# Kernel tuning notes

Measured on AMD Instinct MI355X. Metric: run time of the kernel, lower is better.

Reference implementation:

```python
import jax, jax.numpy as jnp
import numpy as np

N_NODES = 100000
N_EDGES = 800000
N_GRAPHS = 128
BN_EPS = 1e-5


def _bn(h, g, b, m, v):
    # BatchNorm1d in eval mode: uses running stats
    return (h - m) * jax.lax.rsqrt(v + BN_EPS) * g + b


def _gin_layer(x, edge_index, eps, wa, ba, g, be, m, v, wb, bb):
    src, dst = edge_index[0], edge_index[1]
    # sparse neighbor sum: scatter-add messages x[src] into dst
    agg = jax.ops.segment_sum(x[src], dst, num_segments=N_NODES)
    h = (1.0 + eps) * x + agg  # eps shape [1] broadcasts
    h = jax.nn.relu(_bn(h @ wa + ba, g, be, m, v))
    return jax.nn.relu(h @ wb + bb)


def setup_inputs() -> dict:
    key = jax.random.key(0)
    ks = jax.random.split(key, 12)
    inp = {
        'x': jax.random.normal(ks[0], (N_NODES, 384), dtype=jnp.float32),
        'edge_index': jax.random.randint(ks[1], (2, N_EDGES), 0, N_NODES, dtype=jnp.int64),
        'batch': jnp.sort(jax.random.randint(ks[2], (N_NODES,), 0, N_GRAPHS, dtype=jnp.int64)),
        'eps1': jnp.zeros((1,), jnp.float32),
        'w1a': jax.random.normal(ks[3], (384, 128), jnp.float32) * 0.05,
        'b1a': jnp.zeros((128,), jnp.float32),
        'g1': jnp.ones((128,), jnp.float32), 'be1': jnp.zeros((128,), jnp.float32),
        'm1': jnp.zeros((128,), jnp.float32), 'v1': jnp.ones((128,), jnp.float32),
        'w1b': jax.random.normal(ks[4], (128, 128), jnp.float32) * 0.05,
        'b1b': jnp.zeros((128,), jnp.float32),
        'eps2': jnp.zeros((1,), jnp.float32),
        'w2a': jax.random.normal(ks[5], (128, 128), jnp.float32) * 0.05,
        'b2a': jnp.zeros((128,), jnp.float32),
        'g2': jnp.ones((128,), jnp.float32), 'be2': jnp.zeros((128,), jnp.float32),
        'm2': jnp.zeros((128,), jnp.float32), 'v2': jnp.ones((128,), jnp.float32),
        'w2b': jax.random.normal(ks[6], (128, 128), jnp.float32) * 0.05,
        'b2b': jnp.zeros((128,), jnp.float32),
        'eps3': jnp.zeros((1,), jnp.float32),
        'w3a': jax.random.normal(ks[7], (128, 128), jnp.float32) * 0.05,
        'b3a': jnp.zeros((128,), jnp.float32),
        'g3': jnp.ones((128,), jnp.float32), 'be3': jnp.zeros((128,), jnp.float32),
        'm3': jnp.zeros((128,), jnp.float32), 'v3': jnp.ones((128,), jnp.float32),
        'w3b': jax.random.normal(ks[8], (128, 64), jnp.float32) * 0.05,
        'b3b': jnp.zeros((64,), jnp.float32),
        'wc': jax.random.normal(ks[9], (64, 2), jnp.float32) * 0.05,
        'bc': jnp.zeros((2,), jnp.float32),
    }
    return inp


def reference(x, edge_index, batch,
              eps1, w1a, b1a, g1, be1, m1, v1, w1b, b1b,
              eps2, w2a, b2a, g2, be2, m2, v2, w2b, b2b,
              eps3, w3a, b3a, g3, be3, m3, v3, w3b, b3b,
              wc, bc):
    h = _gin_layer(x, edge_index, eps1, w1a, b1a, g1, be1, m1, v1, w1b, b1b)
    # dropout is identity in eval mode
    h = _gin_layer(h, edge_index, eps2, w2a, b2a, g2, be2, m2, v2, w2b, b2b)
    h = _gin_layer(h, edge_index, eps3, w3a, b3a, g3, be3, m3, v3, w3b, b3b)
    # global add pool over graphs
    pooled = jax.ops.segment_sum(h, batch, num_segments=N_GRAPHS)  # [G, 64]
    return pooled @ wc + bc  # [G, num_classes]
```

## Files before the change

### kernel.cpp

```cpp
#include <hip/hip_runtime.h>
#include <hip/hip_bf16.h>


#define N_NODES 100000
#define N_EDGES 800000
#define N_GRAPHS 128
#define NB_SCAN 391
#define LDP 136
#define FLDP 68
#define G1_BLOCKS 1563
#define HIST_BLOCKS 782

typedef __bf16 bf16x8 __attribute__((ext_vector_type(8)));
typedef float f32x4 __attribute__((ext_vector_type(4)));
typedef unsigned short ushort_t;
typedef unsigned int uint_t;

static __device__ __forceinline__ ushort_t f2b(float f) {
    uint_t u = __builtin_bit_cast(uint_t, f);
    uint_t r = (u + 0x7fffu + ((u >> 16) & 1u)) >> 16;
    return (ushort_t)r;
}
static __device__ __forceinline__ float b2f(ushort_t u) {
    return __builtin_bit_cast(float, (uint_t)u << 16);
}

__global__ __launch_bounds__(256) void wt_all_k(
        const float* __restrict__ w1a, const float* __restrict__ w1b,
        const float* __restrict__ w2a, const float* __restrict__ w2b,
        const float* __restrict__ w3a, const float* __restrict__ w3b,
        ushort_t* __restrict__ o1a, ushort_t* __restrict__ o1b,
        ushort_t* __restrict__ o2a, ushort_t* __restrict__ o2b,
        ushort_t* __restrict__ o3a, ushort_t* __restrict__ o3b,
        int* __restrict__ ideg, float* __restrict__ pooled) {
    int t = blockIdx.x * 256 + threadIdx.x;
    if (t < 122880) {
        const float* W; ushort_t* O; int K, N, i;
        if      (t <  49152) { W = w1a; O = o1a; K = 384; N = 128; i = t; }
        else if (t <  65536) { W = w1b; O = o1b; K = 128; N = 128; i = t - 49152; }
        else if (t <  81920) { W = w2a; O = o2a; K = 128; N = 128; i = t - 65536; }
        else if (t <  98304) { W = w2b; O = o2b; K = 128; N = 128; i = t - 81920; }
        else if (t < 114688) { W = w3a; O = o3a; K = 128; N = 128; i = t - 98304; }
        else                 { W = w3b; O = o3b; K = 128; N = 64;  i = t - 114688; }
        int k = i / N, c = i % N;
        O[c * K + k] = f2b(W[i]);
    } else if (t < 222880) {
        ideg[t - 122880] = 0;
    } else if (t < 231072) {
        pooled[t - 222880] = 0.f;
    }
}

__global__ __launch_bounds__(256) void gemm1_hist_k(const float* __restrict__ A,
                                                    const ushort_t* __restrict__ Wt,
                                                    ushort_t* __restrict__ C, int M,
                                                    const int* __restrict__ dst,
                                                    int* __restrict__ deg) {
    __shared__ ushort_t Al[64 * LDP];

    if (blockIdx.x >= G1_BLOCKS) {
        int b = blockIdx.x - G1_BLOCKS;
        int e0 = b * 1024 + threadIdx.x;
        #pragma unroll
        for (int p = 0; p < 4; ++p) {
            int e = e0 + p * 256;
            if (e < N_EDGES) atomicAdd(&deg[dst[e]], 1);
        }
        return;
    }

    constexpr int K = 384;
    const int tid  = threadIdx.x;
    const int lane = tid & 63;
    const int wid  = tid >> 6;
    const int wrow = wid >> 1;
    const int wcol = wid & 1;
    const int l15  = lane & 15;
    const int kg   = lane >> 4;
    const int row0 = blockIdx.x * 64;

    f32x4 acc[2][4];
    #pragma unroll
    for (int i = 0; i < 2; ++i)
        #pragma unroll
        for (int j = 0; j < 4; ++j)
            acc[i][j] = f32x4{0.f, 0.f, 0.f, 0.f};

    const int r  = tid >> 2;
    const int cc = (tid & 3) * 32;

    for (int k0 = 0; k0 < K; k0 += 128) {
        __syncthreads();
        {
            int gr = row0 + r;
            if (gr > M - 1) gr = M - 1;
            const float* pA = A + (size_t)gr * K + k0 + cc;
            float4 v[8];
            #pragma unroll
            for (int p = 0; p < 8; ++p)
                v[p] = *reinterpret_cast<const float4*>(pA + p * 4);
            uint_t u[16];
            #pragma unroll
            for (int p = 0; p < 8; ++p) {
                u[2 * p]     = (uint_t)f2b(v[p].x) | ((uint_t)f2b(v[p].y) << 16);
                u[2 * p + 1] = (uint_t)f2b(v[p].z) | ((uint_t)f2b(v[p].w) << 16);
            }
            uint4* dstp = reinterpret_cast<uint4*>(&Al[r * LDP + cc]);
            dstp[0] = make_uint4(u[0], u[1], u[2], u[3]);
            dstp[1] = make_uint4(u[4], u[5], u[6], u[7]);
            dstp[2] = make_uint4(u[8], u[9], u[10], u[11]);
            dstp[3] = make_uint4(u[12], u[13], u[14], u[15]);
        }
        __syncthreads();

        #pragma unroll
        for (int kk = 0; kk < 4; ++kk) {
            bf16x8 a0 = *reinterpret_cast<const bf16x8*>(&Al[(wrow * 32 + l15) * LDP + kk * 32 + kg * 8]);
            bf16x8 a1 = *reinterpret_cast<const bf16x8*>(&Al[(wrow * 32 + 16 + l15) * LDP + kk * 32 + kg * 8]);
            #pragma unroll
            for (int j = 0; j < 4; ++j) {
                int col = wcol * 64 + j * 16 + l15;
                bf16x8 b = *reinterpret_cast<const bf16x8*>(Wt + (size_t)col * K + k0 + kk * 32 + kg * 8);
                acc[0][j] = __builtin_amdgcn_mfma_f32_16x16x32_bf16(a0, b, acc[0][j], 0, 0, 0);
                acc[1][j] = __builtin_amdgcn_mfma_f32_16x16x32_bf16(a1, b, acc[1][j], 0, 0, 0);
            }
        }
    }

    __syncthreads();
    #pragma unroll
    for (int i = 0; i < 2; ++i)
        #pragma unroll
        for (int j = 0; j < 4; ++j) {
            int col = wcol * 64 + j * 16 + l15;
            #pragma unroll
            for (int q = 0; q < 4; ++q) {
                int row = wrow * 32 + i * 16 + kg * 4 + q;
                Al[row * LDP + col] = f2b(acc[i][j][q]);
            }
        }
    __syncthreads();
    #pragma unroll
    for (int p = 0; p < 4; ++p) {
        int idx = tid + p * 256;
        int rr = idx >> 4, c16 = idx & 15;
        int gr = row0 + rr;
        if (gr < M)
            *reinterpret_cast<uint4*>(C + (size_t)gr * 128 + c16 * 8) =
                *reinterpret_cast<const uint4*>(&Al[rr * LDP + c16 * 8]);
    }
}

__global__ __launch_bounds__(256) void scan1_k(const int* __restrict__ deg,
                                               int* __restrict__ tmp,
                                               int* __restrict__ bsum) {
    __shared__ int s[256];
    int i = blockIdx.x * 256 + threadIdx.x;
    int t = threadIdx.x;
    s[t] = (i < N_NODES) ? deg[i] : 0;
    __syncthreads();
    for (int off = 1; off < 256; off <<= 1) {
        int v = (t >= off) ? s[t - off] : 0;
        __syncthreads();
        s[t] += v;
        __syncthreads();
    }
    if (i < N_NODES) tmp[i] = s[t];
    if (t == 255) bsum[blockIdx.x] = s[255];
}

__global__ __launch_bounds__(256) void scan23_k(const int* __restrict__ tmp,
                                                const int* __restrict__ deg,
                                                const int* __restrict__ bsum,
                                                int* __restrict__ row_start) {
    __shared__ int sb[256];
    int t = threadIdx.x;
    int partial = 0;
    for (int i = t; i < (int)blockIdx.x; i += 256) partial += bsum[i];
    sb[t] = partial;
    __syncthreads();
    for (int off = 128; off > 0; off >>= 1) {
        if (t < off) sb[t] += sb[t + off];
        __syncthreads();
    }
    int boff = sb[0];
    int i = blockIdx.x * 256 + t;
    if (i < N_NODES) row_start[i] = tmp[i] - deg[i] + boff;
}

__global__ __launch_bounds__(256) void fill_k(const int* __restrict__ src,
                                              const int* __restrict__ dst,
                                              int* __restrict__ row_start,
                                              int* __restrict__ csr_src) {
    int e = blockIdx.x * 256 + threadIdx.x;
    if (e >= N_EDGES) return;
    int idx = atomicAdd(&row_start[dst[e]], 1);
    csr_src[idx] = src[e];
}

template<bool TAIL>
__global__ __launch_bounds__(256) void gather_mlp_k(
        const ushort_t* __restrict__ Yin,
        const int* __restrict__ csr, const int* __restrict__ rend,
        const int* __restrict__ deg,
        const float* __restrict__ epsp, const float* __restrict__ ba,
        const float* __restrict__ g, const float* __restrict__ be,
        const float* __restrict__ mm, const float* __restrict__ vv,
        const ushort_t* __restrict__ Wb, const float* __restrict__ bias1,
        const ushort_t* __restrict__ Wa2,
        ushort_t* __restrict__ Yout,
        const int* __restrict__ batch, float* __restrict__ pooled, int M) {
    constexpr int NJ1 = TAIL ? 2 : 4;
    __shared__ ushort_t Hl[64 * LDP];
    __shared__ ushort_t Xl[64 * LDP];
    float* Fl = (float*)Xl;

    const int tid  = threadIdx.x;
    const int lane = tid & 63;
    const int wid  = tid >> 6;
    const int l15  = lane & 15;
    const int slot = lane >> 4;
    const int c0   = l15 * 8;
    const int row0 = blockIdx.x * 64;

    {
        float ep = 1.0f + epsp[0];
        float sc[8], sh[8];
        #pragma unroll
        for (int jj = 0; jj < 8; ++jj) {
            int c = c0 + jj;
            float s = g[c] * rsqrtf(vv[c] + 1e-5f);
            sc[jj] = s;
            sh[jj] = (ba[c] - mm[c]) * s + be[c];
        }

        const int base = row0 + wid * 16;
        int cn = base; if (cn > M - 1) cn = M - 1;
        int end = rend[cn], d = deg[cn];
        int st = end - d;
        int nlim = (d > 64) ? 64 : d;
        int nb = (lane < nlim) ? csr[st + lane] : 0;

        for (int nl = 0; nl < 16; ++nl) {
            int node = base + nl; if (node > M - 1) node = M - 1;
            int nxt = base + nl + 1; if (nxt > M - 1) nxt = M - 1;
            int nend = 0, nd = 0;
            if (nl < 15) { nend = rend[nxt]; nd = deg[nxt]; }

            uint4 ow = *reinterpret_cast<const uint4*>(Yin + (size_t)node * 128 + c0);

            float acc[8] = {0.f, 0.f, 0.f, 0.f, 0.f, 0.f, 0.f, 0.f};
            for (int j0 = 0; j0 < nlim; j0 += 8) {
                int jA = j0 + slot;
                int jB = j0 + 4 + slot;
                int ia = __shfl(nb, jA & 63);
                int ib = __shfl(nb, jB & 63);
                uint4 wa = *reinterpret_cast<const uint4*>(Yin + (size_t)ia * 128 + c0);
                uint4 wb = *reinterpret_cast<const uint4*>(Yin + (size_t)ib * 128 + c0);
                float fa = (jA < nlim) ? 1.f : 0.f;
                float fb = (jB < nlim) ? 1.f : 0.f;
                uint_t ua[4] = {wa.x, wa.y, wa.z, wa.w};
                uint_t ub[4] = {wb.x, wb.y, wb.z, wb.w};
                #pragma unroll
                for (int p = 0; p < 4; ++p) {
                    acc[2 * p]     += fa * b2f((ushort_t)(ua[p] & 0xffff));
                    acc[2 * p + 1] += fa * b2f((ushort_t)(ua[p] >> 16));
                    acc[2 * p]     += fb * b2f((ushort_t)(ub[p] & 0xffff));
                    acc[2 * p + 1] += fb * b2f((ushort_t)(ub[p] >> 16));
                }
            }
            for (int j = st + 64; j < end; ++j) {
                if (slot == 0) {
                    int idx = csr[j];
                    uint4 w = *reinterpret_cast<const uint4*>(Yin + (size_t)idx * 128 + c0);
                    uint_t uw[4] = {w.x, w.y, w.z, w.w};
                    #pragma unroll
                    for (int p = 0; p < 4; ++p) {
                        acc[2 * p]     += b2f((ushort_t)(uw[p] & 0xffff));
                        acc[2 * p + 1] += b2f((ushort_t)(uw[p] >> 16));
                    }
                }
            }

            int nst = nend - nd;
            int nnlim = (nd > 64) ? 64 : nd;
            int nb2 = 0;
            if (nl < 15 && lane < nnlim) nb2 = csr[nst + lane];

            #pragma unroll
            for (int jj = 0; jj < 8; ++jj) {
                acc[jj] += __shfl_xor(acc[jj], 16);
                acc[jj] += __shfl_xor(acc[jj], 32);
            }
            uint_t uo[4] = {ow.x, ow.y, ow.z, ow.w};
            ushort_t rr[8];
            #pragma unroll
            for (int p = 0; p < 4; ++p) {
                float o0 = b2f((ushort_t)(uo[p] & 0xffff));
                float o1 = b2f((ushort_t)(uo[p] >> 16));
                float t0 = sc[2 * p] * (ep * o0 + acc[2 * p]) + sh[2 * p];
                float t1 = sc[2 * p + 1] * (ep * o1 + acc[2 * p + 1]) + sh[2 * p + 1];
                rr[2 * p]     = f2b(fmaxf(t0, 0.f));
                rr[2 * p + 1] = f2b(fmaxf(t1, 0.f));
            }
            if (slot == 0) {
                uint4 packed;
                packed.x = (uint_t)rr[0] | ((uint_t)rr[1] << 16);
                packed.y = (uint_t)rr[2] | ((uint_t)rr[3] << 16);
                packed.z = (uint_t)rr[4] | ((uint_t)rr[5] << 16);
                packed.w = (uint_t)rr[6] | ((uint_t)rr[7] << 16);
                *reinterpret_cast<uint4*>(&Hl[(wid * 16 + nl) * LDP + c0]) = packed;
            }

            end = nend; d = nd; st = nst; nlim = nnlim; nb = nb2;
        }
    }
    __syncthreads();

    const int wrow = wid >> 1;
    const int wcol = wid & 1;
    const int kg   = lane >> 4;

    f32x4 acc1[2][NJ1];
    #pragma unroll
    for (int i = 0; i < 2; ++i)
        #pragma unroll
        for (int j = 0; j < NJ1; ++j)
            acc1[i][j] = f32x4{0.f, 0.f, 0.f, 0.f};
    #pragma unroll
    for (int kk = 0; kk < 4; ++kk) {
        bf16x8 a0 = *reinterpret_cast<const bf16x8*>(&Hl[(wrow * 32 + l15) * LDP + kk * 32 + kg * 8]);
        bf16x8 a1 = *reinterpret_cast<const bf16x8*>(&Hl[(wrow * 32 + 16 + l15) * LDP + kk * 32 + kg * 8]);
        #pragma unroll
        for (int j = 0; j < NJ1; ++j) {
            int col = wcol * (16 * NJ1) + j * 16 + l15;
            bf16x8 b = *reinterpret_cast<const bf16x8*>(Wb + (size_t)col * 128 + kk * 32 + kg * 8);
            acc1[0][j] = __builtin_amdgcn_mfma_f32_16x16x32_bf16(a0, b, acc1[0][j], 0, 0, 0);
            acc1[1][j] = __builtin_amdgcn_mfma_f32_16x16x32_bf16(a1, b, acc1[1][j], 0, 0, 0);
        }
    }

    if constexpr (TAIL) {
        #pragma unroll
        for (int i = 0; i < 2; ++i)
            #pragma unroll
            for (int j = 0; j < NJ1; ++j) {
                int col = wcol * 32 + j * 16 + l15;
                float bi = bias1[col];
                #pragma unroll
                for (int q = 0; q < 4; ++q) {
                    int row = wrow * 32 + i * 16 + kg * 4 + q;
                    Fl[row * FLDP + col] = fmaxf(acc1[i][j][q] + bi, 0.f);
                }
            }
        __syncthreads();
        int col = tid & 63;
        int qq  = tid >> 6;
        float a = 0.f;
        int cur = -1;
        for (int rr2 = 0; rr2 < 16; ++rr2) {
            int r = qq * 16 + rr2;
            int gr = row0 + r;
            if (gr >= M) break;
            int b = batch[gr];
            if (b != cur) {
                if (cur >= 0) atomicAdd(&pooled[cur * 64 + col], a);
                a = 0.f;
                cur = b;
            }
            a += Fl[r * FLDP + col];
        }
        if (cur >= 0) atomicAdd(&pooled[cur * 64 + col], a);
    } else {
        #pragma unroll
        for (int i = 0; i < 2; ++i)
            #pragma unroll
            for (int j = 0; j < NJ1; ++j) {
                int col = wcol * 64 + j * 16 + l15;
                float bi = bias1[col];
                #pragma unroll
                for (int q = 0; q < 4; ++q) {
                    int row = wrow * 32 + i * 16 + kg * 4 + q;
                    Xl[row * LDP + col] = f2b(fmaxf(acc1[i][j][q] + bi, 0.f));
                }
            }
        __syncthreads();

        f32x4 acc2[2][4];
        #pragma unroll
        for (int i = 0; i < 2; ++i)
            #pragma unroll
            for (int j = 0; j < 4; ++j)
                acc2[i][j] = f32x4{0.f, 0.f, 0.f, 0.f};
        #pragma unroll
        for (int kk = 0; kk < 4; ++kk) {
            bf16x8 a0 = *reinterpret_cast<const bf16x8*>(&Xl[(wrow * 32 + l15) * LDP + kk * 32 + kg * 8]);
            bf16x8 a1 = *reinterpret_cast<const bf16x8*>(&Xl[(wrow * 32 + 16 + l15) * LDP + kk * 32 + kg * 8]);
            #pragma unroll
            for (int j = 0; j < 4; ++j) {
                int col = wcol * 64 + j * 16 + l15;
                bf16x8 b = *reinterpret_cast<const bf16x8*>(Wa2 + (size_t)col * 128 + kk * 32 + kg * 8);
                acc2[0][j] = __builtin_amdgcn_mfma_f32_16x16x32_bf16(a0, b, acc2[0][j], 0, 0, 0);
                acc2[1][j] = __builtin_amdgcn_mfma_f32_16x16x32_bf16(a1, b, acc2[1][j], 0, 0, 0);
            }
        }
        __syncthreads();
        #pragma unroll
        for (int i = 0; i < 2; ++i)
            #pragma unroll
            for (int j = 0; j < 4; ++j) {
                int col = wcol * 64 + j * 16 + l15;
                #pragma unroll
                for (int q = 0; q < 4; ++q) {
                    int row = wrow * 32 + i * 16 + kg * 4 + q;
                    Hl[row * LDP + col] = f2b(acc2[i][j][q]);
                }
            }
        __syncthreads();
        #pragma unroll
        for (int p = 0; p < 4; ++p) {
            int idx = tid + p * 256;
            int r = idx >> 4, c16 = idx & 15;
            int gr = row0 + r;
            if (gr < M)
                *reinterpret_cast<uint4*>(Yout + (size_t)gr * 128 + c16 * 8) =
                    *reinterpret_cast<const uint4*>(&Hl[r * LDP + c16 * 8]);
        }
    }
}

__global__ __launch_bounds__(256) void classifier_k(const float* __restrict__ pooled,
                                                    const float* __restrict__ wc,
                                                    const float* __restrict__ bc,
                                                    float* __restrict__ out) {
    int t = threadIdx.x;
    int gidx = t >> 1, c = t & 1;
    float s = bc[c];
    #pragma unroll
    for (int k = 0; k < 64; ++k)
        s += pooled[gidx * 64 + k] * wc[k * 2 + c];
    out[gidx * 2 + c] = s;
}

extern "C" void kernel_launch(void* const* d_in, const int* in_sizes, int n_in,
                              void* d_out, int out_size, void* d_ws, size_t ws_size,
                              hipStream_t stream) {
    const float* x     = (const float*)d_in[0];
    const int*   ei    = (const int*)d_in[1];
    const int*   src   = ei;
    const int*   dst   = ei + N_EDGES;
    const int*   batch = (const int*)d_in[2];
    const float* eps1 = (const float*)d_in[3];
    const float* w1a  = (const float*)d_in[4];
    const float* b1a  = (const float*)d_in[5];
    const float* g1   = (const float*)d_in[6];
    const float* be1  = (const float*)d_in[7];
    const float* m1   = (const float*)d_in[8];
    const float* v1   = (const float*)d_in[9];
    const float* w1b  = (const float*)d_in[10];
    const float* b1b  = (const float*)d_in[11];
    const float* eps2 = (const float*)d_in[12];
    const float* w2a  = (const float*)d_in[13];
    const float* b2a  = (const float*)d_in[14];
    const float* g2   = (const float*)d_in[15];
    const float* be2  = (const float*)d_in[16];
    const float* m2   = (const float*)d_in[17];
    const float* v2   = (const float*)d_in[18];
    const float* w2b  = (const float*)d_in[19];
    const float* b2b  = (const float*)d_in[20];
    const float* eps3 = (const float*)d_in[21];
    const float* w3a  = (const float*)d_in[22];
    const float* b3a  = (const float*)d_in[23];
    const float* g3   = (const float*)d_in[24];
    const float* be3  = (const float*)d_in[25];
    const float* m3   = (const float*)d_in[26];
    const float* v3   = (const float*)d_in[27];
    const float* w3b  = (const float*)d_in[28];
    const float* b3b  = (const float*)d_in[29];
    const float* wc   = (const float*)d_in[30];
    const float* bc   = (const float*)d_in[31];
    float* out = (float*)d_out;

    ushort_t* Y = (ushort_t*)d_ws;
    ushort_t* H = Y + 12800000;
    ushort_t* wt1a = H + 12800000;
    ushort_t* wt1b = wt1a + 49152;
    ushort_t* wt2a = wt1b + 16384;
    ushort_t* wt2b = wt2a + 16384;
    ushort_t* wt3a = wt2b + 16384;
    ushort_t* wt3b = wt3a + 16384;
    float* pooled = (float*)(wt3b + 8192);
    int* ideg = (int*)(pooled + 8192);
    int* irow = ideg + N_NODES;
    int* itmp = irow + N_NODES;
    int* icsr = itmp + N_NODES;
    int* ibsum = icsr + N_EDGES;

    const int M = N_NODES;
    const int gGemm = (M + 63) / 64;
    const int gEdge = (N_EDGES + 255) / 256;
    const int gNode = NB_SCAN;

    wt_all_k<<<903, 256, 0, stream>>>(w1a, w1b, w2a, w2b, w3a, w3b,
                                      wt1a, wt1b, wt2a, wt2b, wt3a, wt3b,
                                      ideg, pooled);

    gemm1_hist_k<<<G1_BLOCKS + HIST_BLOCKS, 256, 0, stream>>>(x, wt1a, Y, M, dst, ideg);

    scan1_k<<<gNode, 256, 0, stream>>>(ideg, itmp, ibsum);
    scan23_k<<<gNode, 256, 0, stream>>>(itmp, ideg, ibsum, irow);
    fill_k<<<gEdge, 256, 0, stream>>>(src, dst, irow, icsr);

    gather_mlp_k<false><<<gGemm, 256, 0, stream>>>(
        Y, icsr, irow, ideg, eps1, b1a, g1, be1, m1, v1,
        wt1b, b1b, wt2a, H, nullptr, nullptr, M);
    gather_mlp_k<false><<<gGemm, 256, 0, stream>>>(
        H, icsr, irow, ideg, eps2, b2a, g2, be2, m2, v2,
        wt2b, b2b, wt3a, Y, nullptr, nullptr, M);
    gather_mlp_k<true><<<gGemm, 256, 0, stream>>>(
        Y, icsr, irow, ideg, eps3, b3a, g3, be3, m3, v3,
        wt3b, b3b, nullptr, nullptr, batch, pooled, M);

    classifier_k<<<1, 256, 0, stream>>>(pooled, wc, bc, out);
}
```

Measured before the change: 359.1 us.

## Double-buffer gemm1 A tiles with async global-to-LDS loads and swizzle

The first-layer GEMM now streams fp32 A tiles straight into LDS with global_load_lds, double-buffered over six 64-wide K steps, so the next tile's load overlaps the current MFMA work. Conversion to bf16 moves to the LDS read side, and an XOR swizzle on 16-byte chunks is meant to avoid bank conflicts. The goal is to hide global load latency and drop the register round trip and one barrier per step. In exchange LDS use doubles (fp32, two buffers), which may lower occupancy, and each wave repeats the fp32-to-bf16 conversions on every LDS read.

```diff
diff --git a/kernel.cpp b/kernel.cpp
--- a/kernel.cpp
+++ b/kernel.cpp
@@ -23,6 +23,12 @@
 }
 static __device__ __forceinline__ float b2f(ushort_t u) {
     return __builtin_bit_cast(float, (uint_t)u << 16);
+}
+
+static __device__ __forceinline__ void gload_lds16(const float* gp, float* lp) {
+    __builtin_amdgcn_global_load_lds(
+        (const __attribute__((address_space(1))) void*)gp,
+        (__attribute__((address_space(3))) void*)lp, 16, 0, 0);
 }
 
 __global__ __launch_bounds__(256) void wt_all_k(
@@ -56,7 +62,7 @@
                                                     ushort_t* __restrict__ C, int M,
                                                     const int* __restrict__ dst,
                                                     int* __restrict__ deg) {
-    __shared__ ushort_t Al[64 * LDP];
+    __shared__ float Af[2][64 * 64];
 
     if (blockIdx.x >= G1_BLOCKS) {
         int b = blockIdx.x - G1_BLOCKS;
@@ -79,6 +85,16 @@
     const int kg   = lane >> 4;
     const int row0 = blockIdx.x * 64;
 
+    const int Rb = wid * 4 + (lane >> 4);
+    int grs[4]; int css[4];
+    #pragma unroll
+    for (int p = 0; p < 4; ++p) {
+        int R = p * 16 + Rb;
+        int gr = row0 + R; if (gr > M - 1) gr = M - 1;
+        grs[p] = gr;
+        css[p] = (lane & 15) ^ (R & 7);
+    }
+
     f32x4 acc[2][4];
     #pragma unroll
     for (int i = 0; i < 2; ++i)
@@ -86,48 +102,53 @@
         for (int j = 0; j < 4; ++j)
             acc[i][j] = f32x4{0.f, 0.f, 0.f, 0.f};
 
-    const int r  = tid >> 2;
-    const int cc = (tid & 3) * 32;
-
-    for (int k0 = 0; k0 < K; k0 += 128) {
-        __syncthreads();
-        {
-            int gr = row0 + r;
-            if (gr > M - 1) gr = M - 1;
-            const float* pA = A + (size_t)gr * K + k0 + cc;
-            float4 v[8];
-            #pragma unroll
-            for (int p = 0; p < 8; ++p)
-                v[p] = *reinterpret_cast<const float4*>(pA + p * 4);
-            uint_t u[16];
-            #pragma unroll
-            for (int p = 0; p < 8; ++p) {
-                u[2 * p]     = (uint_t)f2b(v[p].x) | ((uint_t)f2b(v[p].y) << 16);
-                u[2 * p + 1] = (uint_t)f2b(v[p].z) | ((uint_t)f2b(v[p].w) << 16);
-            }
-            uint4* dstp = reinterpret_cast<uint4*>(&Al[r * LDP + cc]);
-            dstp[0] = make_uint4(u[0], u[1], u[2], u[3]);
-            dstp[1] = make_uint4(u[4], u[5], u[6], u[7]);
-            dstp[2] = make_uint4(u[8], u[9], u[10], u[11]);
-            dstp[3] = make_uint4(u[12], u[13], u[14], u[15]);
-        }
-        __syncthreads();
-
-        #pragma unroll
-        for (int kk = 0; kk < 4; ++kk) {
-            bf16x8 a0 = *reinterpret_cast<const bf16x8*>(&Al[(wrow * 32 + l15) * LDP + kk * 32 + kg * 8]);
-            bf16x8 a1 = *reinterpret_cast<const bf16x8*>(&Al[(wrow * 32 + 16 + l15) * LDP + kk * 32 + kg * 8]);
+    #pragma unroll
+    for (int p = 0; p < 4; ++p)
+        gload_lds16(A + (size_t)grs[p] * K + 0 + css[p] * 4,
+                    &Af[0][p * 1024 + wid * 256]);
+    __syncthreads();
+
+    int cur = 0;
+    const int rA0 = wrow * 32 + l15;
+    const int rA1 = wrow * 32 + 16 + l15;
+    const int s0 = rA0 & 7, s1 = rA1 & 7;
+
+    #pragma unroll
+    for (int t = 0; t < 6; ++t) {
+        if (t < 5) {
+            int k0n = (t + 1) * 64;
+            #pragma unroll
+            for (int p = 0; p < 4; ++p)
+                gload_lds16(A + (size_t)grs[p] * K + k0n + css[p] * 4,
+                            &Af[cur ^ 1][p * 1024 + wid * 256]);
+        }
+        const float* B0 = &Af[cur][rA0 * 64];
+        const float* B1 = &Af[cur][rA1 * 64];
+        #pragma unroll
+        for (int kk = 0; kk < 2; ++kk) {
+            int u0 = kk * 8 + kg * 2;
+            float4 lo0 = *reinterpret_cast<const float4*>(B0 + ((u0) ^ s0) * 4);
+            float4 hi0 = *reinterpret_cast<const float4*>(B0 + ((u0 + 1) ^ s0) * 4);
+            float4 lo1 = *reinterpret_cast<const float4*>(B1 + ((u0) ^ s1) * 4);
+            float4 hi1 = *reinterpret_cast<const float4*>(B1 + ((u0 + 1) ^ s1) * 4);
+            bf16x8 a0, a1;
+            a0[0] = (__bf16)lo0.x; a0[1] = (__bf16)lo0.y; a0[2] = (__bf16)lo0.z; a0[3] = (__bf16)lo0.w;
+            a0[4] = (__bf16)hi0.x; a0[5] = (__bf16)hi0.y; a0[6] = (__bf16)hi0.z; a0[7] = (__bf16)hi0.w;
+            a1[0] = (__bf16)lo1.x; a1[1] = (__bf16)lo1.y; a1[2] = (__bf16)lo1.z; a1[3] = (__bf16)lo1.w;
+            a1[4] = (__bf16)hi1.x; a1[5] = (__bf16)hi1.y; a1[6] = (__bf16)hi1.z; a1[7] = (__bf16)hi1.w;
             #pragma unroll
             for (int j = 0; j < 4; ++j) {
                 int col = wcol * 64 + j * 16 + l15;
-                bf16x8 b = *reinterpret_cast<const bf16x8*>(Wt + (size_t)col * K + k0 + kk * 32 + kg * 8);
+                bf16x8 b = *reinterpret_cast<const bf16x8*>(Wt + (size_t)col * K + t * 64 + kk * 32 + kg * 8);
                 acc[0][j] = __builtin_amdgcn_mfma_f32_16x16x32_bf16(a0, b, acc[0][j], 0, 0, 0);
                 acc[1][j] = __builtin_amdgcn_mfma_f32_16x16x32_bf16(a1, b, acc[1][j], 0, 0, 0);
             }
         }
-    }
-
-    __syncthreads();
+        __syncthreads();
+        cur ^= 1;
+    }
+
+    ushort_t* Es = (ushort_t*)&Af[0][0];
     #pragma unroll
     for (int i = 0; i < 2; ++i)
         #pragma unroll
@@ -136,7 +157,7 @@
             #pragma unroll
             for (int q = 0; q < 4; ++q) {
                 int row = wrow * 32 + i * 16 + kg * 4 + q;
-                Al[row * LDP + col] = f2b(acc[i][j][q]);
+                Es[row * LDP + col] = f2b(acc[i][j][q]);
             }
         }
     __syncthreads();
@@ -147,7 +168,7 @@
         int gr = row0 + rr;
         if (gr < M)
             *reinterpret_cast<uint4*>(C + (size_t)gr * 128 + c16 * 8) =
-                *reinterpret_cast<const uint4*>(&Al[rr * LDP + c16 * 8]);
+                *reinterpret_cast<const uint4*>(&Es[rr * LDP + c16 * 8]);
     }
 }
 
```

Measured after the change: 353.7 us. No clear change (-1.5%).

## Stream fp32 GEMM1 input directly to LDS and use 512-thread gather blocks

Applied to the files above, without the earlier changes.

The first-layer GEMM now loads the fp32 input tile straight into LDS with global_load_lds. It uses 32-row tiles with an XOR swizzle and converts to bf16 when building MFMA operands, instead of converting in registers before the LDS store. This aims to cut register pressure and VGPR round-trips on the bandwidth-heavy 384-wide input read, at the cost of twice as many blocks, each doing half the MFMA work per B-fragment load. The gather/MLP kernels move to 512-thread blocks with 8 nodes per wave instead of 16, raising wave-level parallelism for the irregular neighbour gathers. Each wave now holds 16 rows instead of 32 in its MFMA tiles, which lowers reuse of the weight fragments it loads.

```diff
diff --git a/kernel.cpp b/kernel.cpp
--- a/kernel.cpp
+++ b/kernel.cpp
@@ -8,7 +8,7 @@
 #define NB_SCAN 391
 #define LDP 136
 #define FLDP 68
-#define G1_BLOCKS 1563
+#define G1_BLOCKS 3125
 #define HIST_BLOCKS 782
 
 typedef __bf16 bf16x8 __attribute__((ext_vector_type(8)));
@@ -23,6 +23,12 @@
 }
 static __device__ __forceinline__ float b2f(ushort_t u) {
     return __builtin_bit_cast(float, (uint_t)u << 16);
+}
+
+static __device__ __forceinline__ void gload16(const void* gp, void* lp) {
+    __builtin_amdgcn_global_load_lds(
+        (const __attribute__((address_space(1))) void*)gp,
+        (__attribute__((address_space(3))) void*)lp, 16, 0, 0);
 }
 
 __global__ __launch_bounds__(256) void wt_all_k(
@@ -56,7 +62,7 @@
                                                     ushort_t* __restrict__ C, int M,
                                                     const int* __restrict__ dst,
                                                     int* __restrict__ deg) {
-    __shared__ ushort_t Al[64 * LDP];
+    __shared__ __align__(16) float Al[32 * 384];
 
     if (blockIdx.x >= G1_BLOCKS) {
         int b = blockIdx.x - G1_BLOCKS;
@@ -77,77 +83,62 @@
     const int wcol = wid & 1;
     const int l15  = lane & 15;
     const int kg   = lane >> 4;
-    const int row0 = blockIdx.x * 64;
-
-    f32x4 acc[2][4];
-    #pragma unroll
-    for (int i = 0; i < 2; ++i)
-        #pragma unroll
-        for (int j = 0; j < 4; ++j)
-            acc[i][j] = f32x4{0.f, 0.f, 0.f, 0.f};
-
-    const int r  = tid >> 2;
-    const int cc = (tid & 3) * 32;
-
-    for (int k0 = 0; k0 < K; k0 += 128) {
-        __syncthreads();
-        {
-            int gr = row0 + r;
-            if (gr > M - 1) gr = M - 1;
-            const float* pA = A + (size_t)gr * K + k0 + cc;
-            float4 v[8];
-            #pragma unroll
-            for (int p = 0; p < 8; ++p)
-                v[p] = *reinterpret_cast<const float4*>(pA + p * 4);
-            uint_t u[16];
-            #pragma unroll
-            for (int p = 0; p < 8; ++p) {
-                u[2 * p]     = (uint_t)f2b(v[p].x) | ((uint_t)f2b(v[p].y) << 16);
-                u[2 * p + 1] = (uint_t)f2b(v[p].z) | ((uint_t)f2b(v[p].w) << 16);
-            }
-            uint4* dstp = reinterpret_cast<uint4*>(&Al[r * LDP + cc]);
-            dstp[0] = make_uint4(u[0], u[1], u[2], u[3]);
-            dstp[1] = make_uint4(u[4], u[5], u[6], u[7]);
-            dstp[2] = make_uint4(u[8], u[9], u[10], u[11]);
-            dstp[3] = make_uint4(u[12], u[13], u[14], u[15]);
-        }
-        __syncthreads();
-
-        #pragma unroll
-        for (int kk = 0; kk < 4; ++kk) {
-            bf16x8 a0 = *reinterpret_cast<const bf16x8*>(&Al[(wrow * 32 + l15) * LDP + kk * 32 + kg * 8]);
-            bf16x8 a1 = *reinterpret_cast<const bf16x8*>(&Al[(wrow * 32 + 16 + l15) * LDP + kk * 32 + kg * 8]);
-            #pragma unroll
-            for (int j = 0; j < 4; ++j) {
-                int col = wcol * 64 + j * 16 + l15;
-                bf16x8 b = *reinterpret_cast<const bf16x8*>(Wt + (size_t)col * K + k0 + kk * 32 + kg * 8);
-                acc[0][j] = __builtin_amdgcn_mfma_f32_16x16x32_bf16(a0, b, acc[0][j], 0, 0, 0);
-                acc[1][j] = __builtin_amdgcn_mfma_f32_16x16x32_bf16(a1, b, acc[1][j], 0, 0, 0);
-            }
-        }
-    }
-
+    const int row0 = blockIdx.x * 32;
+
+    #pragma unroll
+    for (int p = 0; p < 12; ++p) {
+        int unit = tid + p * 256;
+        int r  = unit / 96;
+        int cu = unit % 96;
+        int cs = cu ^ (r & 7);
+        gload16(A + (size_t)(row0 + r) * K + cs * 4, &Al[unit * 4]);
+    }
     __syncthreads();
-    #pragma unroll
-    for (int i = 0; i < 2; ++i)
+
+    f32x4 acc[4];
+    #pragma unroll
+    for (int j = 0; j < 4; ++j) acc[j] = f32x4{0.f, 0.f, 0.f, 0.f};
+
+    const int rA = wrow * 16 + l15;
+    const int sw = rA & 7;
+    const float* Arow = &Al[rA * 384];
+
+    #pragma unroll
+    for (int kk = 0; kk < 12; ++kk) {
+        int u = kk * 8 + kg * 2;
+        float4 lo = *reinterpret_cast<const float4*>(Arow + ((u)     ^ sw) * 4);
+        float4 hi = *reinterpret_cast<const float4*>(Arow + ((u + 1) ^ sw) * 4);
+        bf16x8 a;
+        a[0] = (__bf16)lo.x; a[1] = (__bf16)lo.y; a[2] = (__bf16)lo.z; a[3] = (__bf16)lo.w;
+        a[4] = (__bf16)hi.x; a[5] = (__bf16)hi.y; a[6] = (__bf16)hi.z; a[7] = (__bf16)hi.w;
         #pragma unroll
         for (int j = 0; j < 4; ++j) {
             int col = wcol * 64 + j * 16 + l15;
-            #pragma unroll
-            for (int q = 0; q < 4; ++q) {
-                int row = wrow * 32 + i * 16 + kg * 4 + q;
-                Al[row * LDP + col] = f2b(acc[i][j][q]);
-            }
-        }
+            bf16x8 b = *reinterpret_cast<const bf16x8*>(Wt + (size_t)col * K + kk * 32 + kg * 8);
+            acc[j] = __builtin_amdgcn_mfma_f32_16x16x32_bf16(a, b, acc[j], 0, 0, 0);
+        }
+    }
+
     __syncthreads();
-    #pragma unroll
-    for (int p = 0; p < 4; ++p) {
+    ushort_t* Es = (ushort_t*)Al;
+    #pragma unroll
+    for (int j = 0; j < 4; ++j) {
+        int col = wcol * 64 + j * 16 + l15;
+        #pragma unroll
+        for (int q = 0; q < 4; ++q) {
+            int row = wrow * 16 + kg * 4 + q;
+            Es[row * LDP + col] = f2b(acc[j][q]);
+        }
+    }
+    __syncthreads();
+    #pragma unroll
+    for (int p = 0; p < 2; ++p) {
         int idx = tid + p * 256;
         int rr = idx >> 4, c16 = idx & 15;
         int gr = row0 + rr;
         if (gr < M)
             *reinterpret_cast<uint4*>(C + (size_t)gr * 128 + c16 * 8) =
-                *reinterpret_cast<const uint4*>(&Al[rr * LDP + c16 * 8]);
+                *reinterpret_cast<const uint4*>(&Es[rr * LDP + c16 * 8]);
     }
 }
 
@@ -199,7 +190,7 @@
 }
 
 template<bool TAIL>
-__global__ __launch_bounds__(256) void gather_mlp_k(
+__global__ __launch_bounds__(512) void gather_mlp_k(
         const ushort_t* __restrict__ Yin,
         const int* __restrict__ csr, const int* __restrict__ rend,
         const int* __restrict__ deg,
@@ -234,18 +225,18 @@
             sh[jj] = (ba[c] - mm[c]) * s + be[c];
         }
 
-        const int base = row0 + wid * 16;
+        const int base = row0 + wid * 8;
         int cn = base; if (cn > M - 1) cn = M - 1;
         int end = rend[cn], d = deg[cn];
         int st = end - d;
         int nlim = (d > 64) ? 64 : d;
         int nb = (lane < nlim) ? csr[st + lane] : 0;
 
-        for (int nl = 0; nl < 16; ++nl) {
+        for (int nl = 0; nl < 8; ++nl) {
             int node = base + nl; if (node > M - 1) node = M - 1;
             int nxt = base + nl + 1; if (nxt > M - 1) nxt = M - 1;
             int nend = 0, nd = 0;
-            if (nl < 15) { nend = rend[nxt]; nd = deg[nxt]; }
+            if (nl < 7) { nend = rend[nxt]; nd = deg[nxt]; }
 
             uint4 ow = *reinterpret_cast<const uint4*>(Yin + (size_t)node * 128 + c0);
 
@@ -285,7 +276,7 @@
             int nst = nend - nd;
             int nnlim = (nd > 64) ? 64 : nd;
             int nb2 = 0;
-            if (nl < 15 && lane < nnlim) nb2 = csr[nst + lane];
+            if (nl < 7 && lane < nnlim) nb2 = csr[nst + lane];
 
             #pragma unroll
             for (int jj = 0; jj < 8; ++jj) {
@@ -309,7 +300,7 @@
                 packed.y = (uint_t)rr[2] | ((uint_t)rr[3] << 16);
                 packed.z = (uint_t)rr[4] | ((uint_t)rr[5] << 16);
                 packed.w = (uint_t)rr[6] | ((uint_t)rr[7] << 16);
-                *reinterpret_cast<uint4*>(&Hl[(wid * 16 + nl) * LDP + c0]) = packed;
+                *reinterpret_cast<uint4*>(&Hl[(wid * 8 + nl) * LDP + c0]) = packed;
             }
 
             end = nend; d = nd; st = nst; nlim = nnlim; nb = nb2;
@@ -321,45 +312,38 @@
     const int wcol = wid & 1;
     const int kg   = lane >> 4;
 
-    f32x4 acc1[2][NJ1];
-    #pragma unroll
-    for (int i = 0; i < 2; ++i)
-        #pragma unroll
-        for (int j = 0; j < NJ1; ++j)
-            acc1[i][j] = f32x4{0.f, 0.f, 0.f, 0.f};
+    f32x4 acc1[NJ1];
+    #pragma unroll
+    for (int j = 0; j < NJ1; ++j) acc1[j] = f32x4{0.f, 0.f, 0.f, 0.f};
     #pragma unroll
     for (int kk = 0; kk < 4; ++kk) {
-        bf16x8 a0 = *reinterpret_cast<const bf16x8*>(&Hl[(wrow * 32 + l15) * LDP + kk * 32 + kg * 8]);
-        bf16x8 a1 = *reinterpret_cast<const bf16x8*>(&Hl[(wrow * 32 + 16 + l15) * LDP + kk * 32 + kg * 8]);
+        bf16x8 a = *reinterpret_cast<const bf16x8*>(&Hl[(wrow * 16 + l15) * LDP + kk * 32 + kg * 8]);
         #pragma unroll
         for (int j = 0; j < NJ1; ++j) {
             int col = wcol * (16 * NJ1) + j * 16 + l15;
             bf16x8 b = *reinterpret_cast<const bf16x8*>(Wb + (size_t)col * 128 + kk * 32 + kg * 8);
-            acc1[0][j] = __builtin_amdgcn_mfma_f32_16x16x32_bf16(a0, b, acc1[0][j], 0, 0, 0);
-            acc1[1][j] = __builtin_amdgcn_mfma_f32_16x16x32_bf16(a1, b, acc1[1][j], 0, 0, 0);
+            acc1[j] = __builtin_amdgcn_mfma_f32_16x16x32_bf16(a, b, acc1[j], 0, 0, 0);
         }
     }
 
     if constexpr (TAIL) {
         #pragma unroll
-        for (int i = 0; i < 2; ++i)
+        for (int j = 0; j < NJ1; ++j) {
+            int col = wcol * 32 + j * 16 + l15;
+            float bi = bias1[col];
             #pragma unroll
-            for (int j = 0; j < NJ1; ++j) {
-                int col = wcol * 32 + j * 16 + l15;
-                float bi = bias1[col];
-                #pragma unroll
-                for (int q = 0; q < 4; ++q) {
-                    int row = wrow * 32 + i * 16 + kg * 4 + q;
-                    Fl[row * FLDP + col] = fmaxf(acc1[i][j][q] + bi, 0.f);
-                }
-            }
+            for (int q = 0; q < 4; ++q) {
+                int row = wrow * 16 + kg * 4 + q;
+                Fl[row * FLDP + col] = fmaxf(acc1[j][q] + bi, 0.f);
+            }
+        }
         __syncthreads();
         int col = tid & 63;
         int qq  = tid >> 6;
         float a = 0.f;
         int cur = -1;
-        for (int rr2 = 0; rr2 < 16; ++rr2) {
-            int r = qq * 16 + rr2;
+        for (int rr2 = 0; rr2 < 8; ++rr2) {
+            int r = qq * 8 + rr2;
             int gr = row0 + r;
             if (gr >= M) break;
             int b = batch[gr];
@@ -373,53 +357,44 @@
         if (cur >= 0) atomicAdd(&pooled[cur * 64 + col], a);
     } else {
         #pragma unroll
-        for (int i = 0; i < 2; ++i)
+        for (int j = 0; j < NJ1; ++j) {
+            int col = wcol * 64 + j * 16 + l15;
+            float bi = bias1[col];
             #pragma unroll
-            for (int j = 0; j < NJ1; ++j) {
-                int col = wcol * 64 + j * 16 + l15;
-                float bi = bias1[col];
-                #pragma unroll
-                for (int q = 0; q < 4; ++q) {
-                    int row = wrow * 32 + i * 16 + kg * 4 + q;
-                    Xl[row * LDP + col] = f2b(fmaxf(acc1[i][j][q] + bi, 0.f));
-                }
-            }
-        __syncthreads();
-
-        f32x4 acc2[2][4];
-        #pragma unroll
-        for (int i = 0; i < 2; ++i)
-            #pragma unroll
-            for (int j = 0; j < 4; ++j)
-                acc2[i][j] = f32x4{0.f, 0.f, 0.f, 0.f};
+            for (int q = 0; q < 4; ++q) {
+                int row = wrow * 16 + kg * 4 + q;
+                Xl[row * LDP + col] = f2b(fmaxf(acc1[j][q] + bi, 0.f));
+            }
+        }
+        __syncthreads();
+
+        f32x4 acc2[4];
+        #pragma unroll
+        for (int j = 0; j < 4; ++j) acc2[j] = f32x4{0.f, 0.f, 0.f, 0.f};
         #pragma unroll
         for (int kk = 0; kk < 4; ++kk) {
-            bf16x8 a0 = *reinterpret_cast<const bf16x8*>(&Xl[(wrow * 32 + l15) * LDP + kk * 32 + kg * 8]);
-            bf16x8 a1 = *reinterpret_cast<const bf16x8*>(&Xl[(wrow * 32 + 16 + l15) * LDP + kk * 32 + kg * 8]);
+            bf16x8 a = *reinterpret_cast<const bf16x8*>(&Xl[(wrow * 16 + l15) * LDP + kk * 32 + kg * 8]);
             #pragma unroll
             for (int j = 0; j < 4; ++j) {
                 int col = wcol * 64 + j * 16 + l15;
                 bf16x8 b = *reinterpret_cast<const bf16x8*>(Wa2 + (size_t)col * 128 + kk * 32 + kg * 8);
-                acc2[0][j] = __builtin_amdgcn_mfma_f32_16x16x32_bf16(a0, b, acc2[0][j], 0, 0, 0);
-                acc2[1][j] = __builtin_amdgcn_mfma_f32_16x16x32_bf16(a1, b, acc2[1][j], 0, 0, 0);
-            }
-        }
-        __syncthreads();
-        #pragma unroll
-        for (int i = 0; i < 2; ++i)
+                acc2[j] = __builtin_amdgcn_mfma_f32_16x16x32_bf16(a, b, acc2[j], 0, 0, 0);
+            }
+        }
+        __syncthreads();
+        #pragma unroll
+        for (int j = 0; j < 4; ++j) {
+            int col = wcol * 64 + j * 16 + l15;
             #pragma unroll
-            for (int j = 0; j < 4; ++j) {
-                int col = wcol * 64 + j * 16 + l15;
-                #pragma unroll
-                for (int q = 0; q < 4; ++q) {
-                    int row = wrow * 32 + i * 16 + kg * 4 + q;
-                    Hl[row * LDP + col] = f2b(acc2[i][j][q]);
-                }
-            }
-        __syncthreads();
-        #pragma unroll
-        for (int p = 0; p < 4; ++p) {
-            int idx = tid + p * 256;
+            for (int q = 0; q < 4; ++q) {
+                int row = wrow * 16 + kg * 4 + q;
+                Hl[row * LDP + col] = f2b(acc2[j][q]);
+            }
+        }
+        __syncthreads();
+        #pragma unroll
+        for (int p = 0; p < 2; ++p) {
+            int idx = tid + p * 512;
             int r = idx >> 4, c16 = idx & 15;
             int gr = row0 + r;
             if (gr < M)
@@ -497,7 +472,7 @@
     int* ibsum = icsr + N_EDGES;
 
     const int M = N_NODES;
-    const int gGemm = (M + 63) / 64;
+    const int gLayer = (M + 63) / 64;
     const int gEdge = (N_EDGES + 255) / 256;
     const int gNode = NB_SCAN;
 
@@ -511,13 +486,13 @@
     scan23_k<<<gNode, 256, 0, stream>>>(itmp, ideg, ibsum, irow);
     fill_k<<<gEdge, 256, 0, stream>>>(src, dst, irow, icsr);
 
-    gather_mlp_k<false><<<gGemm, 256, 0, stream>>>(
+    gather_mlp_k<false><<<gLayer, 512, 0, stream>>>(
         Y, icsr, irow, ideg, eps1, b1a, g1, be1, m1, v1,
         wt1b, b1b, wt2a, H, nullptr, nullptr, M);
-    gather_mlp_k<false><<<gGemm, 256, 0, stream>>>(
+    gather_mlp_k<false><<<gLayer, 512, 0, stream>>>(
         H, icsr, irow, ideg, eps2, b2a, g2, be2, m2, v2,
         wt2b, b2b, wt3a, Y, nullptr, nullptr, M);
-    gather_mlp_k<true><<<gGemm, 256, 0, stream>>>(
+    gather_mlp_k<true><<<gLayer, 512, 0, stream>>>(
         Y, icsr, irow, ideg, eps3, b3a, g3, be3, m3, v3,
         wt3b, b3b, nullptr, nullptr, batch, pooled, M);
 
```

Result: slower. 410.6 us (+14.4%).

## Regroup setup kernels: fuse histogram with weight prep, scan1 with GEMM1, 128-row tiles

Applied to the files above, without the earlier changes.

The degree histogram moves into the weight-transpose kernel, and ideg is zeroed with a memset beforehand. The first-pass block scan becomes extra blocks of the first GEMM, which removes one kernel launch. The first GEMM tile grows from 64 to 128 rows per block, so each weight fragment is reused across four MFMA row tiles. The cost is more registers and shared memory per block, which may lower occupancy.

```diff
diff --git a/kernel.cpp b/kernel.cpp
--- a/kernel.cpp
+++ b/kernel.cpp
@@ -8,8 +8,9 @@
 #define NB_SCAN 391
 #define LDP 136
 #define FLDP 68
-#define G1_BLOCKS 1563
+#define G1_BLOCKS 782
 #define HIST_BLOCKS 782
+#define WT_BLOCKS 512
 
 typedef __bf16 bf16x8 __attribute__((ext_vector_type(8)));
 typedef float f32x4 __attribute__((ext_vector_type(4)));
@@ -25,14 +26,25 @@
     return __builtin_bit_cast(float, (uint_t)u << 16);
 }
 
-__global__ __launch_bounds__(256) void wt_all_k(
+__global__ __launch_bounds__(256) void wt_hist_k(
         const float* __restrict__ w1a, const float* __restrict__ w1b,
         const float* __restrict__ w2a, const float* __restrict__ w2b,
         const float* __restrict__ w3a, const float* __restrict__ w3b,
         ushort_t* __restrict__ o1a, ushort_t* __restrict__ o1b,
         ushort_t* __restrict__ o2a, ushort_t* __restrict__ o2b,
         ushort_t* __restrict__ o3a, ushort_t* __restrict__ o3b,
-        int* __restrict__ ideg, float* __restrict__ pooled) {
+        float* __restrict__ pooled,
+        const int* __restrict__ dst, int* __restrict__ ideg) {
+    if (blockIdx.x >= WT_BLOCKS) {
+        int b = blockIdx.x - WT_BLOCKS;
+        int e0 = b * 1024 + threadIdx.x;
+        #pragma unroll
+        for (int p = 0; p < 4; ++p) {
+            int e = e0 + p * 256;
+            if (e < N_EDGES) atomicAdd(&ideg[dst[e]], 1);
+        }
+        return;
+    }
     int t = blockIdx.x * 256 + threadIdx.x;
     if (t < 122880) {
         const float* W; ushort_t* O; int K, N, i;
@@ -44,28 +56,34 @@
         else                 { W = w3b; O = o3b; K = 128; N = 64;  i = t - 114688; }
         int k = i / N, c = i % N;
         O[c * K + k] = f2b(W[i]);
-    } else if (t < 222880) {
-        ideg[t - 122880] = 0;
-    } else if (t < 231072) {
-        pooled[t - 222880] = 0.f;
-    }
-}
-
-__global__ __launch_bounds__(256) void gemm1_hist_k(const float* __restrict__ A,
-                                                    const ushort_t* __restrict__ Wt,
-                                                    ushort_t* __restrict__ C, int M,
-                                                    const int* __restrict__ dst,
-                                                    int* __restrict__ deg) {
-    __shared__ ushort_t Al[64 * LDP];
+    } else if (t < 131072) {
+        pooled[t - 122880] = 0.f;
+    }
+}
+
+__global__ __launch_bounds__(256) void gemm1_scan1_k(const float* __restrict__ A,
+                                                     const ushort_t* __restrict__ Wt,
+                                                     ushort_t* __restrict__ C, int M,
+                                                     const int* __restrict__ deg,
+                                                     int* __restrict__ tmp,
+                                                     int* __restrict__ bsum) {
+    __shared__ ushort_t Al[128 * LDP];
 
     if (blockIdx.x >= G1_BLOCKS) {
         int b = blockIdx.x - G1_BLOCKS;
-        int e0 = b * 1024 + threadIdx.x;
-        #pragma unroll
-        for (int p = 0; p < 4; ++p) {
-            int e = e0 + p * 256;
-            if (e < N_EDGES) atomicAdd(&deg[dst[e]], 1);
-        }
+        int* s = (int*)Al;
+        int i = b * 256 + threadIdx.x;
+        int t = threadIdx.x;
+        s[t] = (i < N_NODES) ? deg[i] : 0;
+        __syncthreads();
+        for (int off = 1; off < 256; off <<= 1) {
+            int v = (t >= off) ? s[t - off] : 0;
+            __syncthreads();
+            s[t] += v;
+            __syncthreads();
+        }
+        if (i < N_NODES) tmp[i] = s[t];
+        if (t == 255) bsum[b] = s[255];
         return;
     }
 
@@ -77,17 +95,17 @@
     const int wcol = wid & 1;
     const int l15  = lane & 15;
     const int kg   = lane >> 4;
-    const int row0 = blockIdx.x * 64;
-
-    f32x4 acc[2][4];
+    const int row0 = blockIdx.x * 128;
+
+    f32x4 acc[4][4];
     #pragma unroll
-    for (int i = 0; i < 2; ++i)
+    for (int i = 0; i < 4; ++i)
         #pragma unroll
         for (int j = 0; j < 4; ++j)
             acc[i][j] = f32x4{0.f, 0.f, 0.f, 0.f};
 
-    const int r  = tid >> 2;
-    const int cc = (tid & 3) * 32;
+    const int r  = tid >> 1;
+    const int cc = (tid & 1) * 64;
 
     for (int k0 = 0; k0 < K; k0 += 128) {
         __syncthreads();
@@ -95,53 +113,60 @@
             int gr = row0 + r;
             if (gr > M - 1) gr = M - 1;
             const float* pA = A + (size_t)gr * K + k0 + cc;
-            float4 v[8];
-            #pragma unroll
-            for (int p = 0; p < 8; ++p)
-                v[p] = *reinterpret_cast<const float4*>(pA + p * 4);
-            uint_t u[16];
-            #pragma unroll
-            for (int p = 0; p < 8; ++p) {
-                u[2 * p]     = (uint_t)f2b(v[p].x) | ((uint_t)f2b(v[p].y) << 16);
-                u[2 * p + 1] = (uint_t)f2b(v[p].z) | ((uint_t)f2b(v[p].w) << 16);
-            }
-            uint4* dstp = reinterpret_cast<uint4*>(&Al[r * LDP + cc]);
-            dstp[0] = make_uint4(u[0], u[1], u[2], u[3]);
-            dstp[1] = make_uint4(u[4], u[5], u[6], u[7]);
-            dstp[2] = make_uint4(u[8], u[9], u[10], u[11]);
-            dstp[3] = make_uint4(u[12], u[13], u[14], u[15]);
+            #pragma unroll
+            for (int h = 0; h < 2; ++h) {
+                float4 v[8];
+                #pragma unroll
+                for (int p = 0; p < 8; ++p)
+                    v[p] = *reinterpret_cast<const float4*>(pA + h * 32 + p * 4);
+                uint_t u[16];
+                #pragma unroll
+                for (int p = 0; p < 8; ++p) {
+                    u[2 * p]     = (uint_t)f2b(v[p].x) | ((uint_t)f2b(v[p].y) << 16);
+                    u[2 * p + 1] = (uint_t)f2b(v[p].z) | ((uint_t)f2b(v[p].w) << 16);
+                }
+                uint4* dstp = reinterpret_cast<uint4*>(&Al[r * LDP + cc + h * 32]);
+                dstp[0] = make_uint4(u[0], u[1], u[2], u[3]);
+                dstp[1] = make_uint4(u[4], u[5], u[6], u[7]);
+                dstp[2] = make_uint4(u[8], u[9], u[10], u[11]);
+                dstp[3] = make_uint4(u[12], u[13], u[14], u[15]);
+            }
         }
         __syncthreads();
 
         #pragma unroll
         for (int kk = 0; kk < 4; ++kk) {
-            bf16x8 a0 = *reinterpret_cast<const bf16x8*>(&Al[(wrow * 32 + l15) * LDP + kk * 32 + kg * 8]);
-            bf16x8 a1 = *reinterpret_cast<const bf16x8*>(&Al[(wrow * 32 + 16 + l15) * LDP + kk * 32 + kg * 8]);
+            bf16x8 a[4];
+            #pragma unroll
+            for (int i = 0; i < 4; ++i)
+                a[i] = *reinterpret_cast<const bf16x8*>(
+                    &Al[(wrow * 64 + i * 16 + l15) * LDP + kk * 32 + kg * 8]);
             #pragma unroll
             for (int j = 0; j < 4; ++j) {
                 int col = wcol * 64 + j * 16 + l15;
                 bf16x8 b = *reinterpret_cast<const bf16x8*>(Wt + (size_t)col * K + k0 + kk * 32 + kg * 8);
-                acc[0][j] = __builtin_amdgcn_mfma_f32_16x16x32_bf16(a0, b, acc[0][j], 0, 0, 0);
-                acc[1][j] = __builtin_amdgcn_mfma_f32_16x16x32_bf16(a1, b, acc[1][j], 0, 0, 0);
+                #pragma unroll
+                for (int i = 0; i < 4; ++i)
+                    acc[i][j] = __builtin_amdgcn_mfma_f32_16x16x32_bf16(a[i], b, acc[i][j], 0, 0, 0);
             }
         }
     }
 
     __syncthreads();
     #pragma unroll
-    for (int i = 0; i < 2; ++i)
+    for (int i = 0; i < 4; ++i)
         #pragma unroll
         for (int j = 0; j < 4; ++j) {
             int col = wcol * 64 + j * 16 + l15;
             #pragma unroll
             for (int q = 0; q < 4; ++q) {
-                int row = wrow * 32 + i * 16 + kg * 4 + q;
+                int row = wrow * 64 + i * 16 + kg * 4 + q;
                 Al[row * LDP + col] = f2b(acc[i][j][q]);
             }
         }
     __syncthreads();
     #pragma unroll
-    for (int p = 0; p < 4; ++p) {
+    for (int p = 0; p < 8; ++p) {
         int idx = tid + p * 256;
         int rr = idx >> 4, c16 = idx & 15;
         int gr = row0 + rr;
@@ -149,24 +174,6 @@
             *reinterpret_cast<uint4*>(C + (size_t)gr * 128 + c16 * 8) =
                 *reinterpret_cast<const uint4*>(&Al[rr * LDP + c16 * 8]);
     }
-}
-
-__global__ __launch_bounds__(256) void scan1_k(const int* __restrict__ deg,
-                                               int* __restrict__ tmp,
-                                               int* __restrict__ bsum) {
-    __shared__ int s[256];
-    int i = blockIdx.x * 256 + threadIdx.x;
-    int t = threadIdx.x;
-    s[t] = (i < N_NODES) ? deg[i] : 0;
-    __syncthreads();
-    for (int off = 1; off < 256; off <<= 1) {
-        int v = (t >= off) ? s[t - off] : 0;
-        __syncthreads();
-        s[t] += v;
-        __syncthreads();
-    }
-    if (i < N_NODES) tmp[i] = s[t];
-    if (t == 255) bsum[blockIdx.x] = s[255];
 }
 
 __global__ __launch_bounds__(256) void scan23_k(const int* __restrict__ tmp,
@@ -497,27 +504,29 @@
     int* ibsum = icsr + N_EDGES;
 
     const int M = N_NODES;
-    const int gGemm = (M + 63) / 64;
+    const int gLayer = (M + 63) / 64;
     const int gEdge = (N_EDGES + 255) / 256;
     const int gNode = NB_SCAN;
 
-    wt_all_k<<<903, 256, 0, stream>>>(w1a, w1b, w2a, w2b, w3a, w3b,
-                                      wt1a, wt1b, wt2a, wt2b, wt3a, wt3b,
-                                      ideg, pooled);
-
-    gemm1_hist_k<<<G1_BLOCKS + HIST_BLOCKS, 256, 0, stream>>>(x, wt1a, Y, M, dst, ideg);
-
-    scan1_k<<<gNode, 256, 0, stream>>>(ideg, itmp, ibsum);
+    hipMemsetAsync(ideg, 0, N_NODES * sizeof(int), stream);
+    wt_hist_k<<<WT_BLOCKS + HIST_BLOCKS, 256, 0, stream>>>(
+        w1a, w1b, w2a, w2b, w3a, w3b,
+        wt1a, wt1b, wt2a, wt2b, wt3a, wt3b,
+        pooled, dst, ideg);
+
+    gemm1_scan1_k<<<G1_BLOCKS + NB_SCAN, 256, 0, stream>>>(
+        x, wt1a, Y, M, ideg, itmp, ibsum);
+
     scan23_k<<<gNode, 256, 0, stream>>>(itmp, ideg, ibsum, irow);
     fill_k<<<gEdge, 256, 0, stream>>>(src, dst, irow, icsr);
 
-    gather_mlp_k<false><<<gGemm, 256, 0, stream>>>(
+    gather_mlp_k<false><<<gLayer, 256, 0, stream>>>(
         Y, icsr, irow, ideg, eps1, b1a, g1, be1, m1, v1,
         wt1b, b1b, wt2a, H, nullptr, nullptr, M);
-    gather_mlp_k<false><<<gGemm, 256, 0, stream>>>(
+    gather_mlp_k<false><<<gLayer, 256, 0, stream>>>(
         H, icsr, irow, ideg, eps2, b2a, g2, be2, m2, v2,
         wt2b, b2b, wt3a, Y, nullptr, nullptr, M);
-    gather_mlp_k<true><<<gGemm, 256, 0, stream>>>(
+    gather_mlp_k<true><<<gLayer, 256, 0, stream>>>(
         Y, icsr, irow, ideg, eps3, b3a, g3, be3, m3, v3,
         wt3b, b3b, nullptr, nullptr, batch, pooled, M);
 
```

Result: slower. 372.8 us (+3.8%).
